# Kernel tuning notes

Hardware: AMD Instinct MI355X
Metric: run time of the kernel (lower is better)

Reference implementation:

```python
import jax, jax.numpy as jnp
import numpy as np

# Hyperparameters matching the torch module instantiation
STRIDE = (2, 2, 2)
PADDING = (1, 1, 1)
OUTPUT_PADDING = (1, 1, 1)
DILATION = (2, 2, 2)
KERNEL = (3, 3, 3)


def setup_inputs() -> dict:
    key = jax.random.key(0)
    k1, k2, k3 = jax.random.split(key, 3)
    x = jax.random.normal(k1, (2, 64, 32, 32, 32), dtype=jnp.float32)
    # torch ConvTranspose3d weight layout: (C_in, C_out//groups, kD, kH, kW)
    weight = jax.random.normal(k2, (64, 32, 3, 3, 3), dtype=jnp.float32) * 0.05
    bias = jax.random.normal(k3, (32,), dtype=jnp.float32) * 0.05
    return {"x": x, "weight": weight, "bias": bias}


def reference(x, weight, bias):
    # Same math as the naive torch module: zero-insertion upsample by stride,
    # symmetric pad by dilation*(k-1)-padding, dense conv3d with the spatially
    # flipped weight at rhs dilation, trailing output_padding, then bias add.
    # lhs_dilation performs the zero-insertion implicitly (identical result).
    pad = tuple(max(0, d * (k - 1) - p)
                for d, k, p in zip(DILATION, KERNEL, PADDING))
    # (C_in, C_out, k,k,k) -> (C_out, C_in, k,k,k), flipped spatially
    w = jnp.flip(jnp.transpose(weight, (1, 0, 2, 3, 4)), axis=(2, 3, 4))
    out = jax.lax.conv_general_dilated(
        x, w,
        window_strides=(1, 1, 1),
        padding=[(p, p) for p in pad],
        lhs_dilation=STRIDE,
        rhs_dilation=DILATION,
        dimension_numbers=("NCDHW", "OIDHW", "NCDHW"),
    )
    opd, oph, opw = OUTPUT_PADDING
    out = jnp.pad(out, ((0, 0), (0, 0), (0, opd), (0, oph), (0, opw)))
    return out + bias[None, :, None, None, None]
```

## Files before the change

### kernel.cpp

```cpp
#include <hip/hip_runtime.h>


#define DOUT 66
#define CH_SZ (DOUT*DOUT*DOUT)
#define PL    (DOUT*DOUT)

typedef _Float16 half8 __attribute__((ext_vector_type(8)));
typedef float    floatx16 __attribute__((ext_vector_type(16)));

__global__ void w_transpose(const float* __restrict__ w, _Float16* __restrict__ wT) {
    int o = blockIdx.x * 256 + threadIdx.x;
    if (o >= 27 * 32 * 64) return;
    int ci = o & 63, co = (o >> 6) & 31, tap = o >> 11;
    wT[o] = (_Float16)w[ci * (32 * 27) + co * 27 + tap];
}

#define BIAS_TOT4 (2*32*34*(PL/4))
__global__ void bias_planes(const float* __restrict__ bias, float4* __restrict__ out4_unused,
                            float* __restrict__ out) {
    const int tid = threadIdx.x;
    const unsigned base = blockIdx.x * 4096u;
    #pragma unroll
    for (int j = 0; j < 16; ++j) {
        unsigned idx = base + j * 256u + tid;
        if (idx >= BIAS_TOT4) continue;
        unsigned pl = idx / 1089u;
        unsigned slot = idx - pl * 1089u;
        unsigned e  = pl % 34u;
        unsigned nc = pl / 34u;
        unsigned od = (e < 33u) ? 2u * e : 65u;
        float v = bias[nc & 31u];
        float4* p = (float4*)(out + ((size_t)nc * DOUT + od) * PL);
        p[slot] = make_float4(v, v, v, v);
    }
}

__global__ void __launch_bounds__(256, 2) convt_mfma(
    const float* __restrict__ x, const _Float16* __restrict__ wT,
    const float* __restrict__ bias, float* __restrict__ out)
{
    __shared__ unsigned int xlds[18 * 34 * 32];

    const int tid  = threadIdx.x;
    const int lane = tid & 63;
    const int wv   = tid >> 6;

    unsigned b   = blockIdx.x;
    unsigned xcd = b & 7u, li = b >> 3;
    const int dp  = li & 31;
    const int q   = li >> 5;
    const int n   = xcd & 1;
    const int hpt = ((xcd >> 1) << 1) + q;
    const int hpb = hpt * 4;

    for (int i = tid; i < 1152; i += 256) {
        int row = i >> 6, rem = i & 63;
        int iwl = (rem >> 5) * 33, slot = rem & 31;
        xlds[(row * 34 + iwl) * 32 + slot] = 0;
    }

    const float* xn = x + (size_t)n * (64 * 32768);
    const int l32 = tid & 31;
    const int G   = tid >> 5;
    const float* xg = xn + (size_t)(8 * G) * 32768 + l32;

    #pragma unroll
    for (int idl = 0; idl < 3; ++idl) {
        const int id = dp - 1 + idl;
        const bool idv = (unsigned)id < 32u;
        #pragma unroll
        for (int ihl = 0; ihl < 6; ++ihl) {
            const int ih = hpb - 1 + ihl;
            const bool rv = idv && ((unsigned)ih < 32u);
            const int row = idl * 6 + ihl;
            float f[8] = {0.f, 0.f, 0.f, 0.f, 0.f, 0.f, 0.f, 0.f};
            if (rv) {
                const float* xr = xg + (id * 32 + ih) * 32;
                #pragma unroll
                for (int j = 0; j < 8; ++j) f[j] = xr[(size_t)j * 32768];
            }
            uint4 pk;
            pk.x = __builtin_bit_cast(unsigned int, __builtin_amdgcn_cvt_pkrtz(f[0], f[1]));
            pk.y = __builtin_bit_cast(unsigned int, __builtin_amdgcn_cvt_pkrtz(f[2], f[3]));
            pk.z = __builtin_bit_cast(unsigned int, __builtin_amdgcn_cvt_pkrtz(f[4], f[5]));
            pk.w = __builtin_bit_cast(unsigned int, __builtin_amdgcn_cvt_pkrtz(f[6], f[7]));
            const int sp = row * 34 + (l32 + 1);
            *(uint4*)&xlds[sp * 32 + ((G ^ (sp & 7)) << 2)] = pk;
        }
    }
    __syncthreads();

    const int wp    = lane & 31;
    const int khalf = lane >> 5;
    const _Float16* wbase = wT + (lane & 31) * 64 + khalf * 8;

    floatx16 acc = {};
    #pragma unroll 1
    for (int t9 = 0; t9 < 9; ++t9) {
        const int kd = t9 / 3, kh = t9 - 3 * kd;
        const int row = (2 - kd) * 6 + (wv + 2 - kh);
        #pragma unroll
        for (int kw = 0; kw < 3; ++kw) {
            const int sp  = row * 34 + (wp + 2 - kw);
            const int sp7 = sp & 7;
            const unsigned int* xrow = xlds + sp * 32;
            const _Float16* wt = wbase + (t9 * 3 + kw) * 2048;
            #pragma unroll
            for (int cc = 0; cc < 4; ++cc) {
                const int g = cc * 2 + khalf;
                uint4 bu = *(const uint4*)(xrow + ((g ^ sp7) << 2));
                uint4 au = *(const uint4*)(wt + cc * 16);
                acc = __builtin_amdgcn_mfma_f32_32x32x16_f16(
                    __builtin_bit_cast(half8, au),
                    __builtin_bit_cast(half8, bu), acc, 0, 0, 0);
            }
        }
    }

    const int od = 2 * dp + 1;
    const int hp = hpb + wv;
    const int oh_odd = 2 * hp + 1, oh_even = 2 * hp;
    const bool tailrows = (hpt == 7) && (wv == 3);
    #pragma unroll
    for (int r = 0; r < 16; ++r) {
        const int co = (r & 3) + 8 * (r >> 2) + 4 * khalf;
        const float bv = bias[co];
        float* pbase = out + ((size_t)(n * 32 + co) * DOUT + od) * PL;
        float2* orow = (float2*)(pbase + oh_odd * DOUT);
        float2* erow = (float2*)(pbase + oh_even * DOUT);
        orow[wp] = make_float2(bv, acc[r] + bv);
        erow[wp] = make_float2(bv, bv);
        if (wp == 31) {
            orow[32] = make_float2(bv, bv);
            erow[32] = make_float2(bv, bv);
        }
        if (tailrows) {
            float2* t0 = (float2*)(pbase + 64 * DOUT);
            float2* t1 = (float2*)(pbase + 65 * DOUT);
            t0[wp] = make_float2(bv, bv);
            t1[wp] = make_float2(bv, bv);
            if (wp == 31) { t0[32] = make_float2(bv, bv); t1[32] = make_float2(bv, bv); }
        }
    }
}

extern "C" void kernel_launch(void* const* d_in, const int* in_sizes, int n_in,
                              void* d_out, int out_size, void* d_ws, size_t ws_size,
                              hipStream_t stream) {
    const float* x    = (const float*)d_in[0];
    const float* wgt  = (const float*)d_in[1];
    const float* bias = (const float*)d_in[2];
    float* out = (float*)d_out;
    _Float16* wT = (_Float16*)d_ws;

    w_transpose<<<216, 256, 0, stream>>>(wgt, wT);
    bias_planes<<<(BIAS_TOT4 + 4095) / 4096, 256, 0, stream>>>(bias, nullptr, out);
    convt_mfma<<<512, 256, 0, stream>>>(x, wT, bias, out);
}
```

Measured before the change: 126.2 us.

## Double rows per warp so each weight fragment feeds two MFMAs

Each block now covers 8 h-pair rows instead of 4, and each wave computes two output rows with two accumulators that share one weight-fragment load. The grid halves to 256 blocks, and the x tile in LDS grows to 30 rows with a 10-row halo, moved to dynamic shared memory. This cuts weight reloads and halo staging per output, but leaves fewer blocks than the device's compute units and sets launch bounds to one block per SM, so occupancy and latency hiding drop.

```diff
diff --git a/kernel.cpp b/kernel.cpp
--- a/kernel.cpp
+++ b/kernel.cpp
@@ -2,11 +2,12 @@
 
 
 #define DOUT 66
-#define CH_SZ (DOUT*DOUT*DOUT)
 #define PL    (DOUT*DOUT)
 
 typedef _Float16 half8 __attribute__((ext_vector_type(8)));
 typedef float    floatx16 __attribute__((ext_vector_type(16)));
+
+#define CONV_LDS_BYTES (30*34*32*4)
 
 __global__ void w_transpose(const float* __restrict__ w, _Float16* __restrict__ wT) {
     int o = blockIdx.x * 256 + threadIdx.x;
@@ -16,8 +17,7 @@
 }
 
 #define BIAS_TOT4 (2*32*34*(PL/4))
-__global__ void bias_planes(const float* __restrict__ bias, float4* __restrict__ out4_unused,
-                            float* __restrict__ out) {
+__global__ void bias_planes(const float* __restrict__ bias, float* __restrict__ out) {
     const int tid = threadIdx.x;
     const unsigned base = blockIdx.x * 4096u;
     #pragma unroll
@@ -35,25 +35,24 @@
     }
 }
 
-__global__ void __launch_bounds__(256, 2) convt_mfma(
+__global__ void __launch_bounds__(256, 1) convt_mfma(
     const float* __restrict__ x, const _Float16* __restrict__ wT,
     const float* __restrict__ bias, float* __restrict__ out)
 {
-    __shared__ unsigned int xlds[18 * 34 * 32];
+    extern __shared__ unsigned int xlds[];
 
     const int tid  = threadIdx.x;
     const int lane = tid & 63;
     const int wv   = tid >> 6;
 
     unsigned b   = blockIdx.x;
-    unsigned xcd = b & 7u, li = b >> 3;
-    const int dp  = li & 31;
-    const int q   = li >> 5;
+    unsigned xcd = b & 7u;
     const int n   = xcd & 1;
-    const int hpt = ((xcd >> 1) << 1) + q;
-    const int hpb = hpt * 4;
+    const int hpg = xcd >> 1;
+    const int dp  = b >> 3;
+    const int hpb = hpg * 8;
 
-    for (int i = tid; i < 1152; i += 256) {
+    for (int i = tid; i < 1920; i += 256) {
         int row = i >> 6, rem = i & 63;
         int iwl = (rem >> 5) * 33, slot = rem & 31;
         xlds[(row * 34 + iwl) * 32 + slot] = 0;
@@ -69,10 +68,10 @@
         const int id = dp - 1 + idl;
         const bool idv = (unsigned)id < 32u;
         #pragma unroll
-        for (int ihl = 0; ihl < 6; ++ihl) {
+        for (int ihl = 0; ihl < 10; ++ihl) {
             const int ih = hpb - 1 + ihl;
             const bool rv = idv && ((unsigned)ih < 32u);
-            const int row = idl * 6 + ihl;
+            const int row = idl * 10 + ihl;
             float f[8] = {0.f, 0.f, 0.f, 0.f, 0.f, 0.f, 0.f, 0.f};
             if (rv) {
                 const float* xr = xg + (id * 32 + ih) * 32;
@@ -94,52 +93,62 @@
     const int khalf = lane >> 5;
     const _Float16* wbase = wT + (lane & 31) * 64 + khalf * 8;
 
-    floatx16 acc = {};
+    floatx16 acc0 = {}, acc1 = {};
     #pragma unroll 1
     for (int t9 = 0; t9 < 9; ++t9) {
         const int kd = t9 / 3, kh = t9 - 3 * kd;
-        const int row = (2 - kd) * 6 + (wv + 2 - kh);
+        const int r0 = (2 - kd) * 10 + (2 * wv + 2 - kh);
         #pragma unroll
         for (int kw = 0; kw < 3; ++kw) {
-            const int sp  = row * 34 + (wp + 2 - kw);
-            const int sp7 = sp & 7;
-            const unsigned int* xrow = xlds + sp * 32;
+            const int sp0 = r0 * 34 + (wp + 2 - kw);
+            const int sp1 = sp0 + 34;
+            const unsigned int* x0 = xlds + sp0 * 32;
+            const unsigned int* x1 = xlds + sp1 * 32;
+            const int s07 = sp0 & 7, s17 = sp1 & 7;
             const _Float16* wt = wbase + (t9 * 3 + kw) * 2048;
             #pragma unroll
             for (int cc = 0; cc < 4; ++cc) {
                 const int g = cc * 2 + khalf;
-                uint4 bu = *(const uint4*)(xrow + ((g ^ sp7) << 2));
                 uint4 au = *(const uint4*)(wt + cc * 16);
-                acc = __builtin_amdgcn_mfma_f32_32x32x16_f16(
-                    __builtin_bit_cast(half8, au),
-                    __builtin_bit_cast(half8, bu), acc, 0, 0, 0);
+                uint4 b0 = *(const uint4*)(x0 + ((g ^ s07) << 2));
+                uint4 b1 = *(const uint4*)(x1 + ((g ^ s17) << 2));
+                acc0 = __builtin_amdgcn_mfma_f32_32x32x16_f16(
+                    __builtin_bit_cast(half8, au), __builtin_bit_cast(half8, b0),
+                    acc0, 0, 0, 0);
+                acc1 = __builtin_amdgcn_mfma_f32_32x32x16_f16(
+                    __builtin_bit_cast(half8, au), __builtin_bit_cast(half8, b1),
+                    acc1, 0, 0, 0);
             }
         }
     }
 
     const int od = 2 * dp + 1;
-    const int hp = hpb + wv;
-    const int oh_odd = 2 * hp + 1, oh_even = 2 * hp;
-    const bool tailrows = (hpt == 7) && (wv == 3);
     #pragma unroll
-    for (int r = 0; r < 16; ++r) {
-        const int co = (r & 3) + 8 * (r >> 2) + 4 * khalf;
-        const float bv = bias[co];
-        float* pbase = out + ((size_t)(n * 32 + co) * DOUT + od) * PL;
-        float2* orow = (float2*)(pbase + oh_odd * DOUT);
-        float2* erow = (float2*)(pbase + oh_even * DOUT);
-        orow[wp] = make_float2(bv, acc[r] + bv);
-        erow[wp] = make_float2(bv, bv);
-        if (wp == 31) {
-            orow[32] = make_float2(bv, bv);
-            erow[32] = make_float2(bv, bv);
-        }
-        if (tailrows) {
-            float2* t0 = (float2*)(pbase + 64 * DOUT);
-            float2* t1 = (float2*)(pbase + 65 * DOUT);
-            t0[wp] = make_float2(bv, bv);
-            t1[wp] = make_float2(bv, bv);
-            if (wp == 31) { t0[32] = make_float2(bv, bv); t1[32] = make_float2(bv, bv); }
+    for (int t = 0; t < 2; ++t) {
+        const int hp = hpb + 2 * wv + t;
+        const int oh_odd = 2 * hp + 1, oh_even = 2 * hp;
+        const floatx16& acc = t ? acc1 : acc0;
+        const bool tailrows = (hpg == 3) && (wv == 3) && (t == 1);
+        #pragma unroll
+        for (int r = 0; r < 16; ++r) {
+            const int co = (r & 3) + 8 * (r >> 2) + 4 * khalf;
+            const float bv = bias[co];
+            float* pbase = out + ((size_t)(n * 32 + co) * DOUT + od) * PL;
+            float2* orow = (float2*)(pbase + oh_odd * DOUT);
+            float2* erow = (float2*)(pbase + oh_even * DOUT);
+            orow[wp] = make_float2(bv, acc[r] + bv);
+            erow[wp] = make_float2(bv, bv);
+            if (wp == 31) {
+                orow[32] = make_float2(bv, bv);
+                erow[32] = make_float2(bv, bv);
+            }
+            if (tailrows) {
+                float2* t0 = (float2*)(pbase + 64 * DOUT);
+                float2* t1 = (float2*)(pbase + 65 * DOUT);
+                t0[wp] = make_float2(bv, bv);
+                t1[wp] = make_float2(bv, bv);
+                if (wp == 31) { t0[32] = make_float2(bv, bv); t1[32] = make_float2(bv, bv); }
+            }
         }
     }
 }
@@ -153,7 +162,15 @@
     float* out = (float*)d_out;
     _Float16* wT = (_Float16*)d_ws;
 
+    static bool attr_done = false;
+    if (!attr_done) {
+        hipFuncSetAttribute((const void*)convt_mfma,
+                            hipFuncAttributeMaxDynamicSharedMemorySize,
+                            CONV_LDS_BYTES);
+        attr_done = true;
+    }
+
     w_transpose<<<216, 256, 0, stream>>>(wgt, wT);
-    bias_planes<<<(BIAS_TOT4 + 4095) / 4096, 256, 0, stream>>>(bias, nullptr, out);
-    convt_mfma<<<512, 256, 0, stream>>>(x, wT, bias, out);
+    bias_planes<<<(BIAS_TOT4 + 4095) / 4096, 256, 0, stream>>>(bias, out);
+    convt_mfma<<<256, 256, CONV_LDS_BYTES, stream>>>(x, wT, bias, out);
 }
```

Measured after the change: 122.6 us. 2.8% less time.

## Pre-convert input to padded channel-last fp16 and split K across wave pairs

Applied to the files above, without the earlier changes.

Adds a separate kernel that converts x once into a padded, channel-last fp16 buffer in workspace. The conv kernel then drops its per-block LDS staging (which reloaded the halo from fp32 for each block) and reads B fragments directly from global memory. Each wave now computes two output rows that share one weight fragment, and the channel dimension is split across two waves whose partial sums are combined through LDS. In exchange it adds an extra launch and a global write and read of the fp16 copy, and the MFMA operands now come from global/L2 rather than LDS.

```diff
diff --git a/kernel.cpp b/kernel.cpp
--- a/kernel.cpp
+++ b/kernel.cpp
@@ -2,11 +2,15 @@
 
 
 #define DOUT 66
-#define CH_SZ (DOUT*DOUT*DOUT)
-#define PL    (DOUT*DOUT)
+#define PL (DOUT*DOUT)
 
 typedef _Float16 half8 __attribute__((ext_vector_type(8)));
 typedef float    floatx16 __attribute__((ext_vector_type(16)));
+
+#define X16_N_STRIDE  2228224
+#define X16_ROW       2176
+#define WT_BYTES      110592
+#define X16_OFF       131072
 
 __global__ void w_transpose(const float* __restrict__ w, _Float16* __restrict__ wT) {
     int o = blockIdx.x * 256 + threadIdx.x;
@@ -15,9 +19,44 @@
     wT[o] = (_Float16)w[ci * (32 * 27) + co * 27 + tap];
 }
 
+__global__ void x_to_f16t(const float* __restrict__ x, _Float16* __restrict__ x16) {
+    const int tid = threadIdx.x;
+    const unsigned b = blockIdx.x;
+    const int id  = b & 31;
+    const int ihg = (b >> 5) & 3;
+    const int n   = b >> 7;
+    const int iw  = tid & 31;
+    const int ih  = ihg * 8 + (tid >> 5);
+
+    const float* xr = x + (size_t)n * 2097152 + (id * 32 + ih) * 32 + iw;
+    _Float16* drow = x16 + (size_t)n * X16_N_STRIDE + (id * 32 + ih) * X16_ROW;
+
+    #pragma unroll
+    for (int c0 = 0; c0 < 64; c0 += 16) {
+        float f[16];
+        #pragma unroll
+        for (int j = 0; j < 16; ++j) f[j] = xr[(size_t)(c0 + j) * 32768];
+        unsigned pk[8];
+        #pragma unroll
+        for (int j = 0; j < 8; ++j)
+            pk[j] = __builtin_bit_cast(unsigned,
+                        __builtin_amdgcn_cvt_pkrtz(f[2 * j], f[2 * j + 1]));
+        _Float16* dst = drow + (iw + 1) * 64 + c0;
+        ((uint4*)dst)[0] = make_uint4(pk[0], pk[1], pk[2], pk[3]);
+        ((uint4*)dst)[1] = make_uint4(pk[4], pk[5], pk[6], pk[7]);
+    }
+    if (tid < 128) {
+        const int side = tid >> 6;
+        const int ihq2 = (tid >> 3) & 7;
+        const int q    = tid & 7;
+        _Float16* hz = x16 + (size_t)n * X16_N_STRIDE +
+                       (id * 32 + ihg * 8 + ihq2) * X16_ROW + side * 33 * 64 + q * 8;
+        ((uint4*)hz)[0] = make_uint4(0, 0, 0, 0);
+    }
+}
+
 #define BIAS_TOT4 (2*32*34*(PL/4))
-__global__ void bias_planes(const float* __restrict__ bias, float4* __restrict__ out4_unused,
-                            float* __restrict__ out) {
+__global__ void bias_planes(const float* __restrict__ bias, float* __restrict__ out) {
     const int tid = threadIdx.x;
     const unsigned base = blockIdx.x * 4096u;
     #pragma unroll
@@ -36,110 +75,140 @@
 }
 
 __global__ void __launch_bounds__(256, 2) convt_mfma(
-    const float* __restrict__ x, const _Float16* __restrict__ wT,
+    const _Float16* __restrict__ x16, const _Float16* __restrict__ wT,
     const float* __restrict__ bias, float* __restrict__ out)
 {
-    __shared__ unsigned int xlds[18 * 34 * 32];
+    __shared__ float redu[2][2][16][64];
 
     const int tid  = threadIdx.x;
     const int lane = tid & 63;
     const int wv   = tid >> 6;
-
-    unsigned b   = blockIdx.x;
-    unsigned xcd = b & 7u, li = b >> 3;
-    const int dp  = li & 31;
-    const int q   = li >> 5;
+    const int pair = wv >> 1;
+    const int kseg = wv & 1;
+
+    unsigned b = blockIdx.x;
+    const unsigned xcd = b & 7u;
     const int n   = xcd & 1;
-    const int hpt = ((xcd >> 1) << 1) + q;
-    const int hpb = hpt * 4;
-
-    for (int i = tid; i < 1152; i += 256) {
-        int row = i >> 6, rem = i & 63;
-        int iwl = (rem >> 5) * 33, slot = rem & 31;
-        xlds[(row * 34 + iwl) * 32 + slot] = 0;
-    }
-
-    const float* xn = x + (size_t)n * (64 * 32768);
-    const int l32 = tid & 31;
-    const int G   = tid >> 5;
-    const float* xg = xn + (size_t)(8 * G) * 32768 + l32;
-
-    #pragma unroll
-    for (int idl = 0; idl < 3; ++idl) {
-        const int id = dp - 1 + idl;
-        const bool idv = (unsigned)id < 32u;
-        #pragma unroll
-        for (int ihl = 0; ihl < 6; ++ihl) {
-            const int ih = hpb - 1 + ihl;
-            const bool rv = idv && ((unsigned)ih < 32u);
-            const int row = idl * 6 + ihl;
-            float f[8] = {0.f, 0.f, 0.f, 0.f, 0.f, 0.f, 0.f, 0.f};
-            if (rv) {
-                const float* xr = xg + (id * 32 + ih) * 32;
+    const int dp  = (b >> 3) & 31;
+    const int hq  = b >> 8;
+    const int hpg = (int)(((xcd >> 1) << 1) | hq);
+    const int hp0 = hpg * 4 + pair * 2;
+
+    const int wp  = lane & 31;
+    const int kh8 = (lane >> 5) * 8;
+
+    const _Float16* wtl = wT + (lane & 31) * 64 + kseg * 32 + kh8;
+    const _Float16* xb = x16 + (size_t)n * X16_N_STRIDE + wp * 64 + kseg * 32 + kh8;
+
+    floatx16 a0 = {}, a1 = {};
+
+    if (dp >= 1 && dp <= 30 && hp0 >= 1 && hp0 <= 29) {
+        #pragma unroll 3
+        for (int t9 = 0; t9 < 9; ++t9) {
+            const int kd = t9 / 3, kh = t9 % 3;
+            const _Float16* bp0 = xb + ((dp + 1 - kd) * 32 + (hp0 + 1 - kh)) * X16_ROW;
+            const _Float16* wt = wtl + t9 * 3 * 2048;
+            #pragma unroll
+            for (int kw = 0; kw < 3; ++kw) {
+                const int off = (2 - kw) * 64;
                 #pragma unroll
-                for (int j = 0; j < 8; ++j) f[j] = xr[(size_t)j * 32768];
-            }
-            uint4 pk;
-            pk.x = __builtin_bit_cast(unsigned int, __builtin_amdgcn_cvt_pkrtz(f[0], f[1]));
-            pk.y = __builtin_bit_cast(unsigned int, __builtin_amdgcn_cvt_pkrtz(f[2], f[3]));
-            pk.z = __builtin_bit_cast(unsigned int, __builtin_amdgcn_cvt_pkrtz(f[4], f[5]));
-            pk.w = __builtin_bit_cast(unsigned int, __builtin_amdgcn_cvt_pkrtz(f[6], f[7]));
-            const int sp = row * 34 + (l32 + 1);
-            *(uint4*)&xlds[sp * 32 + ((G ^ (sp & 7)) << 2)] = pk;
+                for (int cc = 0; cc < 2; ++cc) {
+                    uint4 au  = *(const uint4*)(wt + kw * 2048 + cc * 16);
+                    uint4 bu0 = *(const uint4*)(bp0 + off + cc * 16);
+                    uint4 bu1 = *(const uint4*)(bp0 + X16_ROW + off + cc * 16);
+                    a0 = __builtin_amdgcn_mfma_f32_32x32x16_f16(
+                        __builtin_bit_cast(half8, au), __builtin_bit_cast(half8, bu0),
+                        a0, 0, 0, 0);
+                    a1 = __builtin_amdgcn_mfma_f32_32x32x16_f16(
+                        __builtin_bit_cast(half8, au), __builtin_bit_cast(half8, bu1),
+                        a1, 0, 0, 0);
+                }
+            }
+        }
+    } else {
+        #pragma unroll 1
+        for (int t9 = 0; t9 < 9; ++t9) {
+            const int kd = t9 / 3, kh = t9 % 3;
+            const int id = dp + 1 - kd;
+            if ((unsigned)id >= 32u) continue;
+            const int ih0 = hp0 + 1 - kh;
+            const bool v0 = (unsigned)ih0 < 32u;
+            const bool v1 = (unsigned)(ih0 + 1) < 32u;
+            const _Float16* bp0 = xb + (id * 32 + ih0) * X16_ROW;
+            const _Float16* wt = wtl + t9 * 3 * 2048;
+            #pragma unroll
+            for (int kw = 0; kw < 3; ++kw) {
+                const int off = (2 - kw) * 64;
+                #pragma unroll
+                for (int cc = 0; cc < 2; ++cc) {
+                    uint4 au = *(const uint4*)(wt + kw * 2048 + cc * 16);
+                    if (v0) {
+                        uint4 bu0 = *(const uint4*)(bp0 + off + cc * 16);
+                        a0 = __builtin_amdgcn_mfma_f32_32x32x16_f16(
+                            __builtin_bit_cast(half8, au), __builtin_bit_cast(half8, bu0),
+                            a0, 0, 0, 0);
+                    }
+                    if (v1) {
+                        uint4 bu1 = *(const uint4*)(bp0 + X16_ROW + off + cc * 16);
+                        a1 = __builtin_amdgcn_mfma_f32_32x32x16_f16(
+                            __builtin_bit_cast(half8, au), __builtin_bit_cast(half8, bu1),
+                            a1, 0, 0, 0);
+                    }
+                }
+            }
+        }
+    }
+
+    if (kseg == 1) {
+        #pragma unroll
+        for (int r = 0; r < 16; ++r) {
+            redu[pair][0][r][lane] = a0[r];
+            redu[pair][1][r][lane] = a1[r];
         }
     }
     __syncthreads();
 
-    const int wp    = lane & 31;
-    const int khalf = lane >> 5;
-    const _Float16* wbase = wT + (lane & 31) * 64 + khalf * 8;
-
-    floatx16 acc = {};
-    #pragma unroll 1
-    for (int t9 = 0; t9 < 9; ++t9) {
-        const int kd = t9 / 3, kh = t9 - 3 * kd;
-        const int row = (2 - kd) * 6 + (wv + 2 - kh);
-        #pragma unroll
-        for (int kw = 0; kw < 3; ++kw) {
-            const int sp  = row * 34 + (wp + 2 - kw);
-            const int sp7 = sp & 7;
-            const unsigned int* xrow = xlds + sp * 32;
-            const _Float16* wt = wbase + (t9 * 3 + kw) * 2048;
-            #pragma unroll
-            for (int cc = 0; cc < 4; ++cc) {
-                const int g = cc * 2 + khalf;
-                uint4 bu = *(const uint4*)(xrow + ((g ^ sp7) << 2));
-                uint4 au = *(const uint4*)(wt + cc * 16);
-                acc = __builtin_amdgcn_mfma_f32_32x32x16_f16(
-                    __builtin_bit_cast(half8, au),
-                    __builtin_bit_cast(half8, bu), acc, 0, 0, 0);
-            }
-        }
-    }
-
     const int od = 2 * dp + 1;
-    const int hp = hpb + wv;
-    const int oh_odd = 2 * hp + 1, oh_even = 2 * hp;
-    const bool tailrows = (hpt == 7) && (wv == 3);
-    #pragma unroll
-    for (int r = 0; r < 16; ++r) {
-        const int co = (r & 3) + 8 * (r >> 2) + 4 * khalf;
-        const float bv = bias[co];
-        float* pbase = out + ((size_t)(n * 32 + co) * DOUT + od) * PL;
-        float2* orow = (float2*)(pbase + oh_odd * DOUT);
-        float2* erow = (float2*)(pbase + oh_even * DOUT);
-        orow[wp] = make_float2(bv, acc[r] + bv);
-        erow[wp] = make_float2(bv, bv);
-        if (wp == 31) {
-            orow[32] = make_float2(bv, bv);
-            erow[32] = make_float2(bv, bv);
-        }
-        if (tailrows) {
-            float2* t0 = (float2*)(pbase + 64 * DOUT);
-            float2* t1 = (float2*)(pbase + 65 * DOUT);
-            t0[wp] = make_float2(bv, bv);
-            t1[wp] = make_float2(bv, bv);
-            if (wp == 31) { t0[32] = make_float2(bv, bv); t1[32] = make_float2(bv, bv); }
+    if (kseg == 0) {
+        #pragma unroll
+        for (int r = 0; r < 16; ++r) {
+            a0[r] += redu[pair][0][r][lane];
+            a1[r] += redu[pair][1][r][lane];
+        }
+        #pragma unroll
+        for (int t = 0; t < 2; ++t) {
+            const int oh = 2 * (hp0 + t) + 1;
+            const floatx16& acc = t ? a1 : a0;
+            #pragma unroll
+            for (int r = 0; r < 16; ++r) {
+                const int co = (r & 3) + 8 * (r >> 2) + 4 * (lane >> 5);
+                const float bv = bias[co];
+                float2* orow = (float2*)(out +
+                    ((size_t)(n * 32 + co) * DOUT + od) * PL + oh * DOUT);
+                orow[wp] = make_float2(bv, acc[r] + bv);
+                if (wp == 31) orow[32] = make_float2(bv, bv);
+            }
+        }
+    } else {
+        const bool tails = (hpg == 7) && (pair == 1);
+        #pragma unroll
+        for (int r = 0; r < 16; ++r) {
+            const int co = (r & 3) + 8 * (r >> 2) + 4 * (lane >> 5);
+            const float bv = bias[co];
+            float* pbase = out + ((size_t)(n * 32 + co) * DOUT + od) * PL;
+            #pragma unroll
+            for (int t = 0; t < 2; ++t) {
+                float2* erow = (float2*)(pbase + (2 * (hp0 + t)) * DOUT);
+                erow[wp] = make_float2(bv, bv);
+                if (wp == 31) erow[32] = make_float2(bv, bv);
+            }
+            if (tails) {
+                float2* t0 = (float2*)(pbase + 64 * DOUT);
+                float2* t1 = (float2*)(pbase + 65 * DOUT);
+                t0[wp] = make_float2(bv, bv);
+                t1[wp] = make_float2(bv, bv);
+                if (wp == 31) { t0[32] = make_float2(bv, bv); t1[32] = make_float2(bv, bv); }
+            }
         }
     }
 }
@@ -151,9 +220,11 @@
     const float* wgt  = (const float*)d_in[1];
     const float* bias = (const float*)d_in[2];
     float* out = (float*)d_out;
-    _Float16* wT = (_Float16*)d_ws;
+    _Float16* wT  = (_Float16*)d_ws;
+    _Float16* x16 = (_Float16*)((char*)d_ws + X16_OFF);
 
     w_transpose<<<216, 256, 0, stream>>>(wgt, wT);
-    bias_planes<<<(BIAS_TOT4 + 4095) / 4096, 256, 0, stream>>>(bias, nullptr, out);
-    convt_mfma<<<512, 256, 0, stream>>>(x, wT, bias, out);
-}
+    x_to_f16t<<<256, 256, 0, stream>>>(x, x16);
+    bias_planes<<<(BIAS_TOT4 + 4095) / 4096, 256, 0, stream>>>(bias, out);
+    convt_mfma<<<512, 256, 0, stream>>>(x16, wT, bias, out);
+}
```

Measured after the change: 137.9 us. 1.09x slower.
